# Kernel tuning notes

Measured on AMD Instinct MI355X. Metric: run time of the kernel, lower is better.

## Reference

```python
import jax, jax.numpy as jnp
import numpy as np

N, E, R = 50000, 400000, 500
X_SIZE = 100
G_SIZE = 100
HID = 64
OUT = 64
HEADS = 2
ALPHA = 0.5
NEG_SLOPE = 0.01  # nn.LeakyReLU default and attention slope
EPS = 1e-12       # F.normalize eps


def _l2norm(x, axis):
    return x / jnp.maximum(jnp.linalg.norm(x, axis=axis, keepdims=True), EPS)


def _xavier(key, shape, gain=1.414):
    fan_in, fan_out = shape[-1], int(np.prod(shape[:-1]))
    std = gain * np.sqrt(2.0 / (fan_in + fan_out))
    return jax.random.normal(key, shape, dtype=jnp.float32) * std


def _att_layer(h, g, row, col, etype, W, b, att, out_size):
    # h: [N, D_h], g: [R, D_g], W: [heads*out, 2*D_h+D_g], att: [1, heads, out]
    n = h.shape[0]
    h_ijk = jnp.concatenate([h[row], h[col], g[etype]], axis=1)      # [E, 2D_h+D_g]
    c_ijk = (h_ijk @ W.T + b).reshape(-1, HEADS, out_size)           # [E, H, O]
    a = jnp.sum(att * c_ijk, axis=2, keepdims=True)                  # [E, H, 1]
    e = jnp.exp(jax.nn.leaky_relu(a, NEG_SLOPE))                     # unnormalized (matches torch exp w/o max-sub)
    denom = jax.ops.segment_sum(e, row, num_segments=n)              # [N, H, 1]
    alpha = e / denom[row]
    # self-edge zeros contribute nothing; segment_sum over num_segments=n is equivalent
    return jax.ops.segment_sum(alpha * c_ijk, col, num_segments=n)   # [N, H, O]


def setup_inputs() -> dict:
    key = jax.random.key(0)
    ks = jax.random.split(key, 20)
    x = jax.random.normal(ks[0], (N, X_SIZE), dtype=jnp.float32)
    g = jax.random.normal(ks[1], (R, G_SIZE), dtype=jnp.float32)
    edge_idx = jax.random.randint(ks[2], (2, E), 0, N)
    edge_type = jax.random.randint(ks[3], (E,), 0, R)
    d1 = 2 * X_SIZE + G_SIZE
    d2 = 2 * HID * HEADS + G_SIZE
    inp = {
        "x": x, "g": g, "edge_idx": edge_idx, "edge_type": edge_type,
        "W1i": _xavier(ks[4], (HEADS * HID, d1)), "b1i": jnp.zeros((HEADS * HID,), jnp.float32),
        "a1i": _xavier(ks[5], (1, HEADS, HID)),
        "W1o": _xavier(ks[6], (HEADS * HID, d1)), "b1o": jnp.zeros((HEADS * HID,), jnp.float32),
        "a1o": _xavier(ks[7], (1, HEADS, HID)),
        "W2i": _xavier(ks[8], (HEADS * OUT, d2)), "b2i": jnp.zeros((HEADS * OUT,), jnp.float32),
        "a2i": _xavier(ks[9], (1, HEADS, OUT)),
        "W2o": _xavier(ks[10], (HEADS * OUT, d2)), "b2o": jnp.zeros((HEADS * OUT,), jnp.float32),
        "a2o": _xavier(ks[11], (1, HEADS, OUT)),
        "We": _xavier(ks[12], (HID, X_SIZE)), "be": jnp.zeros((HID,), jnp.float32),
        "Wr": _xavier(ks[13], (HEADS * HID, G_SIZE)), "br": jnp.zeros((HEADS * HID,), jnp.float32),
    }
    return inp


def reference(x, g, edge_idx, edge_type, W1i, b1i, a1i, W1o, b1o, a1o,
              W2i, b2i, a2i, W2o, b2o, a2o, We, be, Wr, br):
    # x = F.normalize(x, dim=1).detach()
    xn = jax.lax.stop_gradient(_l2norm(x, axis=1))
    row, col = edge_idx[0], edge_idx[1]

    h_in = _att_layer(xn, g, row, col, edge_type, W1i, b1i, a1i, HID)
    h_out = _att_layer(xn, g, col, row, edge_type, W1o, b1o, a1o, HID)
    h = jax.nn.leaky_relu(ALPHA * h_in + (1.0 - ALPHA) * h_out, NEG_SLOPE)
    h = _l2norm(h, axis=2)                                # [N, H, HID]
    h = h.transpose(0, 1, 2).reshape(N, HEADS * HID)      # concat heads

    h_in = _att_layer(h, g, row, col, edge_type, W2i, b2i, a2i, OUT)
    h_out = _att_layer(h, g, col, row, edge_type, W2o, b2o, a2o, OUT)
    h = jax.nn.leaky_relu(ALPHA * h_in + (1.0 - ALPHA) * h_out, NEG_SLOPE)
    h = _l2norm(h, axis=2)                                # [N, H, OUT]

    # EntityLayer: Linear(x)[:, None, :] + h  (requires HID == OUT)
    h_prime = (xn @ We.T + be)[:, None, :] + h            # [N, H, OUT]
    h_prime = h_prime.reshape(N, HEADS * OUT)
    h_prime = _l2norm(h_prime, axis=1)                    # (torch dim=2 bug -> last dim)
    # _merge_heads stores mean but returns input unchanged

    g_prime = g @ Wr.T + br                               # [R, HEADS*HID]
    return h_prime, g_prime
```

## Files before the change

kernel.cpp:

```cpp
#include <hip/hip_runtime.h>

typedef unsigned short u16;
typedef unsigned int u32;
typedef short short8v __attribute__((ext_vector_type(8)));
typedef float float4v __attribute__((ext_vector_type(4)));

#define N_NODES 50000
#define E_EDGES 400000
#define R_REL   500
#define NKEYS   100000
#define SCAN_B  98

__device__ __forceinline__ float bl(u32 u){ return __uint_as_float(u << 16); }
__device__ __forceinline__ float bh(u32 u){ return __uint_as_float(u & 0xffff0000u); }
__device__ __forceinline__ u16 f2b(float f){
    u32 u = __float_as_uint(f);
    return (u16)((u + 0x7fffu + ((u >> 16) & 1u)) >> 16);
}
__device__ __forceinline__ u32 pk2(float a, float b){ return (u32)f2b(a) | ((u32)f2b(b) << 16); }
__device__ __forceinline__ float lrelu(float x){ return x > 0.f ? x : 0.01f * x; }

__global__ void k_norm_x(const float* __restrict__ x, u16* __restrict__ xnb){
    int wid = threadIdx.x >> 6, l = threadIdx.x & 63;
    int n = blockIdx.x * 4 + wid;
    if (n >= N_NODES) return;
    float v0 = x[(size_t)n * 100 + l];
    float v1 = (l + 64 < 100) ? x[(size_t)n * 100 + 64 + l] : 0.f;
    float ss = v0 * v0 + v1 * v1;
    #pragma unroll
    for (int m = 32; m; m >>= 1) ss += __shfl_xor(ss, m);
    float s = 1.f / fmaxf(sqrtf(ss), 1e-12f);
    xnb[(size_t)n * 128 + l] = f2b(v0 * s);
    xnb[(size_t)n * 128 + 64 + l] = (l + 64 < 100) ? f2b(v1 * s) : (u16)0;
}

__global__ void k_build_wcat(const float* __restrict__ W1i, const float* __restrict__ W1o,
                             const float* __restrict__ W2i, const float* __restrict__ W2o,
                             const float* __restrict__ We,
                             u16* __restrict__ wc1, u16* __restrict__ wc2){
    int idx = blockIdx.x * blockDim.x + threadIdx.x;
    if (idx < 576 * 128){
        int r = idx >> 7, k = idx & 127;
        float v = 0.f;
        if (r < 512){
            int seg = r >> 7, rr = r & 127;
            const float* W = (seg < 2) ? W1i : W1o;
            int off = (seg & 1) ? 100 : 0;
            if (k < 100) v = W[(size_t)rr * 300 + off + k];
        } else {
            int rr = r - 512;
            if (k < 100) v = We[(size_t)rr * 100 + k];
        }
        wc1[idx] = f2b(v);
    } else if (idx < 576 * 128 + 512 * 128){
        int j = idx - 576 * 128;
        int r = j >> 7, k = j & 127;
        int seg = r >> 7, rr = r & 127;
        const float* W = (seg < 2) ? W2i : W2o;
        int off = (seg & 1) ? 128 : 0;
        wc2[j] = f2b(W[(size_t)rr * 356 + off + k]);
    }
}

__global__ void k_pg(const float* __restrict__ g,
                     const float* __restrict__ W1i, const float* __restrict__ W1o,
                     const float* __restrict__ W2i, const float* __restrict__ W2o,
                     const float* __restrict__ b1i, const float* __restrict__ b1o,
                     const float* __restrict__ b2i, const float* __restrict__ b2o,
                     const float* __restrict__ a1i, const float* __restrict__ a1o,
                     const float* __restrict__ a2i, const float* __restrict__ a2o,
                     float* __restrict__ Pg, float* __restrict__ qg){
    int bid = blockIdx.x;
    int r = bid >> 2, t = bid & 3;
    const float *W, *b, *att; int ld, off;
    if (t == 0){ W = W1i; ld = 300; off = 200; b = b1i; att = a1i; }
    else if (t == 1){ W = W1o; ld = 300; off = 200; b = b1o; att = a1o; }
    else if (t == 2){ W = W2i; ld = 356; off = 256; b = b2i; att = a2i; }
    else { W = W2o; ld = 356; off = 256; b = b2o; att = a2o; }
    __shared__ float gs[100];
    __shared__ float red[128];
    int j = threadIdx.x;
    if (j < 100) gs[j] = g[(size_t)r * 100 + j];
    __syncthreads();
    float acc = b[j];
    #pragma unroll 4
    for (int k = 0; k < 100; ++k) acc += gs[k] * W[(size_t)j * ld + off + k];
    Pg[((size_t)t * R_REL + r) * 128 + j] = acc;
    red[j] = att[j] * acc;
    __syncthreads();
    if (j < 2){
        float s = 0.f;
        for (int k = 0; k < 64; ++k) s += red[j * 64 + k];
        qg[((size_t)t * R_REL + r) * 2 + j] = s;
    }
}

__global__ void k_gprime(const float* __restrict__ g, const float* __restrict__ Wr,
                         const float* __restrict__ br, float* __restrict__ out){
    int r = blockIdx.x, j = threadIdx.x;
    __shared__ float gs[100];
    if (j < 100) gs[j] = g[(size_t)r * 100 + j];
    __syncthreads();
    float acc = br[j];
    #pragma unroll 4
    for (int k = 0; k < 100; ++k) acc += gs[k] * Wr[(size_t)j * 100 + k];
    out[(size_t)N_NODES * 128 + (size_t)r * 128 + j] = acc;
}

__launch_bounds__(256)
__global__ void k_gemm(const u16* __restrict__ A, const u16* __restrict__ W,
                       u16* __restrict__ C, int M, int NN){
    int l = threadIdx.x & 63, w = threadIdx.x >> 6;
    int rb = blockIdx.x * 64 + w * 16;
    int ar = rb + (l & 15); if (ar >= M) ar = M - 1;
    const u16* Ap = A + (size_t)ar * 128 + (l >> 4) * 8;
    short8v a0 = *(const short8v*)(Ap);
    short8v a1 = *(const short8v*)(Ap + 32);
    short8v a2 = *(const short8v*)(Ap + 64);
    short8v a3 = *(const short8v*)(Ap + 96);
    int ntc = NN >> 4;
    for (int nt = 0; nt < ntc; ++nt){
        const u16* Wp = W + (size_t)(nt * 16 + (l & 15)) * 128 + (l >> 4) * 8;
        short8v b0 = *(const short8v*)(Wp);
        short8v b1 = *(const short8v*)(Wp + 32);
        short8v b2 = *(const short8v*)(Wp + 64);
        short8v b3 = *(const short8v*)(Wp + 96);
        float4v acc = {0.f, 0.f, 0.f, 0.f};
        acc = __builtin_amdgcn_mfma_f32_16x16x32_bf16(a0, b0, acc, 0, 0, 0);
        acc = __builtin_amdgcn_mfma_f32_16x16x32_bf16(a1, b1, acc, 0, 0, 0);
        acc = __builtin_amdgcn_mfma_f32_16x16x32_bf16(a2, b2, acc, 0, 0, 0);
        acc = __builtin_amdgcn_mfma_f32_16x16x32_bf16(a3, b3, acc, 0, 0, 0);
        int cc = nt * 16 + (l & 15);
        int rr0 = rb + (l >> 4) * 4;
        #pragma unroll
        for (int r = 0; r < 4; ++r){
            int rr = rr0 + r;
            if (rr < M) C[(size_t)rr * NN + cc] = f2b(acc[r]);
        }
    }
}

__global__ void k_qnode(const u16* __restrict__ NP, int stride,
                        const float* __restrict__ attI, const float* __restrict__ attO,
                        float* __restrict__ q){
    int wid = threadIdx.x >> 6, l = threadIdx.x & 63;
    int n = blockIdx.x * 4 + wid;
    if (n >= N_NODES) return;
    uint4 uv = *(const uint4*)(NP + (size_t)n * stride + (size_t)l * 8);
    int t = l >> 4, h = (l >> 3) & 1;
    const float* att = ((t < 2) ? attI : attO) + h * 64 + (l & 7) * 8;
    float s = bl(uv.x) * att[0] + bh(uv.x) * att[1] + bl(uv.y) * att[2] + bh(uv.y) * att[3]
            + bl(uv.z) * att[4] + bh(uv.z) * att[5] + bl(uv.w) * att[6] + bh(uv.w) * att[7];
    s += __shfl_xor(s, 1); s += __shfl_xor(s, 2); s += __shfl_xor(s, 4);
    if ((l & 7) == 0) q[(size_t)n * 8 + t * 2 + h] = s;
}

__global__ void k_hist(const int* __restrict__ ei, u32* __restrict__ cnt){
    int e = blockIdx.x * blockDim.x + threadIdx.x;
    if (e >= E_EDGES) return;
    atomicAdd(&cnt[ei[E_EDGES + e]], 1u);
    atomicAdd(&cnt[N_NODES + ei[e]], 1u);
}

__launch_bounds__(1024)
__global__ void k_scan1(const u32* __restrict__ cnt, u32* __restrict__ off, u32* __restrict__ bsum){
    __shared__ u32 sh[1024];
    int t = threadIdx.x, b = blockIdx.x, idx = b * 1024 + t;
    u32 v = cnt[idx];
    sh[t] = v; __syncthreads();
    #pragma unroll
    for (int d = 1; d < 1024; d <<= 1){
        u32 add = (t >= d) ? sh[t - d] : 0;
        __syncthreads();
        sh[t] += add;
        __syncthreads();
    }
    off[idx] = sh[t] - v;
    if (t == 1023) bsum[b] = sh[1023];
}

__global__ void k_scan2(u32* __restrict__ bsum){
    if (threadIdx.x == 0){
        u32 run = 0;
        for (int i = 0; i < SCAN_B; ++i){ u32 t = bsum[i]; bsum[i] = run; run += t; }
    }
}

__launch_bounds__(1024)
__global__ void k_scan3(u32* __restrict__ off, const u32* __restrict__ bsum){
    int idx = blockIdx.x * 1024 + threadIdx.x;
    off[idx] += bsum[blockIdx.x];
}

__global__ void k_pos(const int* __restrict__ ei, const int* __restrict__ ety,
                      u32* __restrict__ cur,
                      u32* __restrict__ Pso, u32* __restrict__ Pss){
    int e = blockIdx.x * blockDim.x + threadIdx.x;
    if (e >= E_EDGES) return;
    u32 row = (u32)ei[e], col = (u32)ei[E_EDGES + e];
    u32 etb = (u32)ety[e] << 20;
    u32 pI = atomicAdd(&cur[col], 1u);
    Pso[pI] = row | etb;  Pss[pI] = col;
    u32 pO = atomicAdd(&cur[N_NODES + row], 1u);
    Pso[pO] = col | etb;  Pss[pO] = row;
}

__global__ void k_edgeA(const u32* __restrict__ Pso, const u32* __restrict__ Pss,
                        const float* __restrict__ q,
                        const float* __restrict__ qgI, const float* __restrict__ qgO,
                        float4* __restrict__ ex){
    int p = blockIdx.x * blockDim.x + threadIdx.x;
    if (p >= 2 * E_EDGES) return;
    u32 so = Pso[p], self = Pss[p];
    u32 oth = so & 0xFFFFF, et = so >> 20;
    u32 row, col;
    if (p < E_EDGES){ row = oth; col = self; } else { row = self; col = oth; }
    const float* qr = q + (size_t)row * 8;
    const float* qc = q + (size_t)col * 8;
    float4 r;
    r.x = expf(lrelu(qr[0] + qc[2] + qgI[(size_t)et * 2 + 0]));
    r.y = expf(lrelu(qr[1] + qc[3] + qgI[(size_t)et * 2 + 1]));
    r.z = expf(lrelu(qc[4] + qr[6] + qgO[(size_t)et * 2 + 0]));
    r.w = expf(lrelu(qc[5] + qr[7] + qgO[(size_t)et * 2 + 1]));
    ex[p] = r;
}

__global__ void k_denom(const u32* __restrict__ off, const float4* __restrict__ ex,
                        float* __restrict__ rdI, float* __restrict__ rdO){
    int n = blockIdx.x * blockDim.x + threadIdx.x;
    if (n >= N_NODES) return;
    float s0 = 0.f, s1 = 0.f;
    for (u32 p = off[N_NODES + n]; p < off[N_NODES + n + 1]; ++p){
        float4 v = ex[p]; s0 += v.x; s1 += v.y;
    }
    rdI[(size_t)n * 2 + 0] = (s0 > 0.f) ? 1.f / s0 : 0.f;
    rdI[(size_t)n * 2 + 1] = (s1 > 0.f) ? 1.f / s1 : 0.f;
    float t0 = 0.f, t1 = 0.f;
    for (u32 p = off[n]; p < off[n + 1]; ++p){
        float4 v = ex[p]; t0 += v.z; t1 += v.w;
    }
    rdO[(size_t)n * 2 + 0] = (t0 > 0.f) ? 1.f / t0 : 0.f;
    rdO[(size_t)n * 2 + 1] = (t1 > 0.f) ? 1.f / t1 : 0.f;
}

__launch_bounds__(256)
__global__ void k_agg(const u32* __restrict__ off,
                      const u32* __restrict__ Pso, const float4* __restrict__ ex,
                      const u16* __restrict__ NP, int stride,
                      const float* __restrict__ PgI, const float* __restrict__ PgO,
                      const float* __restrict__ rdI, const float* __restrict__ rdO,
                      int final_stage,
                      const u16* __restrict__ NP1, const float* __restrict__ be,
                      u16* __restrict__ h1b, float* __restrict__ out){
    int wid = threadIdx.x >> 6, l = threadIdx.x & 63;
    int n = blockIdx.x * 4 + wid;
    if (n >= N_NODES) return;
    int h = l >> 5, d0 = l * 2;
    const u16* selfP = NP + (size_t)n * stride;
    u32 pbi = *(const u32*)(selfP + 128 + d0);
    u32 pbo = *(const u32*)(selfP + 384 + d0);

    float a0 = 0.f, a1 = 0.f, sai = 0.f;
    {
        u32 s0 = off[n], deg = off[n + 1] - s0;
        for (u32 base = 0; base < deg; base += 64){
            u32 k = base + (u32)l;
            u32 so = 0u; float ex0 = 0.f, ex1 = 0.f;
            if (k < deg){
                so = Pso[s0 + k];
                float2 e2 = *(const float2*)((const char*)ex + (size_t)(s0 + k) * 16);
                ex0 = e2.x; ex1 = e2.y;
            }
            int cnt = (int)((deg - base < 64u) ? (deg - base) : 64u);
            for (int c = 0; c < cnt; c += 8){
                float wj[8]; u32 pa[8]; float2 gv[8];
                #pragma unroll
                for (int j = 0; j < 8; ++j){
                    u32 s = __shfl(so, c + j);
                    float e0 = __shfl(ex0, c + j);
                    float e1 = __shfl(ex1, c + j);
                    float e = h ? e1 : e0;
                    u32 oth = s & 0xFFFFFu, et = s >> 20;
                    pa[j] = *(const u32*)(NP + (size_t)oth * stride + d0);
                    gv[j] = *(const float2*)(PgI + (size_t)et * 128 + d0);
                    wj[j] = e * rdI[(size_t)oth * 2 + h];
                }
                #pragma unroll
                for (int j = 0; j < 8; ++j){
                    a0 += wj[j] * (bl(pa[j]) + gv[j].x);
                    a1 += wj[j] * (bh(pa[j]) + gv[j].y);
                    sai += wj[j];
                }
            }
        }
    }
    a0 += sai * bl(pbi);
    a1 += sai * bh(pbi);

    float b0 = 0.f, b1 = 0.f, sao = 0.f;
    {
        u32 s0 = off[N_NODES + n], deg = off[N_NODES + n + 1] - s0;
        for (u32 base = 0; base < deg; base += 64){
            u32 k = base + (u32)l;
            u32 so = 0u; float ex0 = 0.f, ex1 = 0.f;
            if (k < deg){
                so = Pso[s0 + k];
                float2 e2 = *(const float2*)((const char*)ex + (size_t)(s0 + k) * 16 + 8);
                ex0 = e2.x; ex1 = e2.y;
            }
            int cnt = (int)((deg - base < 64u) ? (deg - base) : 64u);
            for (int c = 0; c < cnt; c += 8){
                float wj[8]; u32 pa[8]; float2 gv[8];
                #pragma unroll
                for (int j = 0; j < 8; ++j){
                    u32 s = __shfl(so, c + j);
                    float e0 = __shfl(ex0, c + j);
                    float e1 = __shfl(ex1, c + j);
                    float e = h ? e1 : e0;
                    u32 oth = s & 0xFFFFFu, et = s >> 20;
                    pa[j] = *(const u32*)(NP + (size_t)oth * stride + 256 + d0);
                    gv[j] = *(const float2*)(PgO + (size_t)et * 128 + d0);
                    wj[j] = e * rdO[(size_t)oth * 2 + h];
                }
                #pragma unroll
                for (int j = 0; j < 8; ++j){
                    b0 += wj[j] * (bl(pa[j]) + gv[j].x);
                    b1 += wj[j] * (bh(pa[j]) + gv[j].y);
                    sao += wj[j];
                }
            }
        }
    }
    b0 += sao * bl(pbo);
    b1 += sao * bh(pbo);

    float vx = lrelu(0.5f * (a0 + b0));
    float vy = lrelu(0.5f * (a1 + b1));
    float ss = vx * vx + vy * vy;
    #pragma unroll
    for (int m = 16; m; m >>= 1) ss += __shfl_xor(ss, m);
    float s2 = 1.f / fmaxf(sqrtf(ss), 1e-12f);
    if (!final_stage){
        *(u32*)(h1b + (size_t)n * 128 + d0) = pk2(vx * s2, vy * s2);
    } else {
        float h20 = vx * s2, h21 = vy * s2;
        int o0 = d0 & 63;
        u32 ue = *(const u32*)(NP1 + (size_t)n * 576 + 512 + o0);
        float hp0 = bl(ue) + be[o0] + h20;
        float hp1 = bh(ue) + be[o0 + 1] + h21;
        float st = hp0 * hp0 + hp1 * hp1;
        #pragma unroll
        for (int m = 32; m; m >>= 1) st += __shfl_xor(st, m);
        float s = 1.f / fmaxf(sqrtf(st), 1e-12f);
        float2 o; o.x = hp0 * s; o.y = hp1 * s;
        *(float2*)(out + (size_t)n * 128 + d0) = o;
    }
}

extern "C" void kernel_launch(void* const* d_in, const int* in_sizes, int n_in,
                              void* d_out, int out_size, void* d_ws, size_t ws_size,
                              hipStream_t stream){
    const float* x   = (const float*)d_in[0];
    const float* g   = (const float*)d_in[1];
    const int*   ei  = (const int*)d_in[2];
    const int*   ety = (const int*)d_in[3];
    const float* W1i = (const float*)d_in[4];
    const float* b1i = (const float*)d_in[5];
    const float* a1i = (const float*)d_in[6];
    const float* W1o = (const float*)d_in[7];
    const float* b1o = (const float*)d_in[8];
    const float* a1o = (const float*)d_in[9];
    const float* W2i = (const float*)d_in[10];
    const float* b2i = (const float*)d_in[11];
    const float* a2i = (const float*)d_in[12];
    const float* W2o = (const float*)d_in[13];
    const float* b2o = (const float*)d_in[14];
    const float* a2o = (const float*)d_in[15];
    const float* We  = (const float*)d_in[16];
    const float* be  = (const float*)d_in[17];
    const float* Wr  = (const float*)d_in[18];
    const float* br  = (const float*)d_in[19];
    float* out = (float*)d_out;

    char* ws = (char*)d_ws;
    size_t off_b = 0;
    auto carve = [&](size_t bytes) -> char* {
        char* p = ws + off_b;
        off_b += (bytes + 255) & ~(size_t)255;
        return p;
    };
    u16*    xnb  = (u16*)carve((size_t)N_NODES * 128 * 2);
    u16*    wc1  = (u16*)carve((size_t)576 * 128 * 2);
    u16*    wc2  = (u16*)carve((size_t)512 * 128 * 2);
    u16*    NP1  = (u16*)carve((size_t)N_NODES * 576 * 2);
    u16*    NP2  = (u16*)carve((size_t)N_NODES * 512 * 2);
    u16*    h1b  = (u16*)carve((size_t)N_NODES * 128 * 2);
    float*  q    = (float*)carve((size_t)N_NODES * 8 * 4);
    float*  Pg   = (float*)carve((size_t)4 * R_REL * 128 * 4);
    float*  qg   = (float*)carve((size_t)4 * R_REL * 2 * 4);
    u32*    cnt  = (u32*)carve((size_t)SCAN_B * 1024 * 4);
    u32*    offA = (u32*)carve((size_t)SCAN_B * 1024 * 4);
    u32*    cur  = (u32*)carve((size_t)NKEYS * 4);
    u32*    bsum = (u32*)carve((size_t)SCAN_B * 4);
    u32*    Pso  = (u32*)carve((size_t)2 * E_EDGES * 4);
    u32*    Pss  = (u32*)carve((size_t)2 * E_EDGES * 4);
    float4* ex   = (float4*)carve((size_t)2 * E_EDGES * 16);
    float*  rdI  = (float*)carve((size_t)N_NODES * 2 * 4);
    float*  rdO  = (float*)carve((size_t)N_NODES * 2 * 4);

    hipMemsetAsync(cnt, 0, (size_t)SCAN_B * 1024 * 4, stream);
    k_hist<<<1563, 256, 0, stream>>>(ei, cnt);
    k_scan1<<<SCAN_B, 1024, 0, stream>>>(cnt, offA, bsum);
    k_scan2<<<1, 64, 0, stream>>>(bsum);
    k_scan3<<<SCAN_B, 1024, 0, stream>>>(offA, bsum);
    hipMemcpyAsync(cur, offA, (size_t)NKEYS * 4, hipMemcpyDeviceToDevice, stream);
    k_pos<<<1563, 256, 0, stream>>>(ei, ety, cur, Pso, Pss);

    k_norm_x<<<12500, 256, 0, stream>>>(x, xnb);
    k_build_wcat<<<544, 256, 0, stream>>>(W1i, W1o, W2i, W2o, We, wc1, wc2);
    k_pg<<<2000, 128, 0, stream>>>(g, W1i, W1o, W2i, W2o, b1i, b1o, b2i, b2o,
                                   a1i, a1o, a2i, a2o, Pg, qg);
    k_gprime<<<500, 128, 0, stream>>>(g, Wr, br, out);

    k_gemm<<<782, 256, 0, stream>>>(xnb, wc1, NP1, N_NODES, 576);
    k_qnode<<<12500, 256, 0, stream>>>(NP1, 576, a1i, a1o, q);
    k_edgeA<<<3125, 256, 0, stream>>>(Pso, Pss, q, qg, qg + R_REL * 2, ex);
    k_denom<<<196, 256, 0, stream>>>(offA, ex, rdI, rdO);
    k_agg<<<12500, 256, 0, stream>>>(offA, Pso, ex, NP1, 576, Pg, Pg + R_REL * 128,
                                     rdI, rdO, 0, NP1, be, h1b, out);

    k_gemm<<<782, 256, 0, stream>>>(h1b, wc2, NP2, N_NODES, 512);
    k_qnode<<<12500, 256, 0, stream>>>(NP2, 512, a2i, a2o, q);
    k_edgeA<<<3125, 256, 0, stream>>>(Pso, Pss, q, qg + 2 * R_REL * 2, qg + 3 * R_REL * 2, ex);
    k_denom<<<196, 256, 0, stream>>>(offA, ex, rdI, rdO);
    k_agg<<<12500, 256, 0, stream>>>(offA, Pso, ex, NP2, 512, Pg + 2 * R_REL * 128,
                                     Pg + 3 * R_REL * 128, rdI, rdO, 1, NP1, be, h1b, out);
}
```

Before: 461.0 us.

## Split node projections into per-segment planes and interleave in/out aggregation loops

New measurement: 470.5 us. 1.02x slower.

```diff
diff --git a/kernel.cpp b/kernel.cpp
--- a/kernel.cpp
+++ b/kernel.cpp
@@ -10,6 +10,7 @@
 #define R_REL   500
 #define NKEYS   100000
 #define SCAN_B  98
+#define SEG     ((size_t)N_NODES * 128)
 
 __device__ __forceinline__ float bl(u32 u){ return __uint_as_float(u << 16); }
 __device__ __forceinline__ float bh(u32 u){ return __uint_as_float(u & 0xffff0000u); }
@@ -109,7 +110,7 @@
 
 __launch_bounds__(256)
 __global__ void k_gemm(const u16* __restrict__ A, const u16* __restrict__ W,
-                       u16* __restrict__ C, int M, int NN){
+                       u16* __restrict__ NPt, int M, int NN){
     int l = threadIdx.x & 63, w = threadIdx.x >> 6;
     int rb = blockIdx.x * 64 + w * 16;
     int ar = rb + (l & 15); if (ar >= M) ar = M - 1;
@@ -131,23 +132,27 @@
         acc = __builtin_amdgcn_mfma_f32_16x16x32_bf16(a2, b2, acc, 0, 0, 0);
         acc = __builtin_amdgcn_mfma_f32_16x16x32_bf16(a3, b3, acc, 0, 0, 0);
         int cc = nt * 16 + (l & 15);
+        int seg = cc >> 7;
         int rr0 = rb + (l >> 4) * 4;
         #pragma unroll
         for (int r = 0; r < 4; ++r){
             int rr = rr0 + r;
-            if (rr < M) C[(size_t)rr * NN + cc] = f2b(acc[r]);
+            if (rr < M){
+                if (seg < 4) NPt[(size_t)seg * SEG + (size_t)rr * 128 + (cc & 127)] = f2b(acc[r]);
+                else         NPt[4 * SEG + (size_t)rr * 64 + (cc & 63)] = f2b(acc[r]);
+            }
         }
     }
 }
 
-__global__ void k_qnode(const u16* __restrict__ NP, int stride,
+__global__ void k_qnode(const u16* __restrict__ NPt,
                         const float* __restrict__ attI, const float* __restrict__ attO,
                         float* __restrict__ q){
     int wid = threadIdx.x >> 6, l = threadIdx.x & 63;
     int n = blockIdx.x * 4 + wid;
     if (n >= N_NODES) return;
-    uint4 uv = *(const uint4*)(NP + (size_t)n * stride + (size_t)l * 8);
     int t = l >> 4, h = (l >> 3) & 1;
+    uint4 uv = *(const uint4*)(NPt + (size_t)t * SEG + (size_t)n * 128 + (l & 15) * 8);
     const float* att = ((t < 2) ? attI : attO) + h * 64 + (l & 7) * 8;
     float s = bl(uv.x) * att[0] + bh(uv.x) * att[1] + bl(uv.y) * att[2] + bh(uv.y) * att[3]
             + bl(uv.z) * att[4] + bh(uv.z) * att[5] + bl(uv.w) * att[6] + bh(uv.w) * att[7];
@@ -246,91 +251,96 @@
 __launch_bounds__(256)
 __global__ void k_agg(const u32* __restrict__ off,
                       const u32* __restrict__ Pso, const float4* __restrict__ ex,
-                      const u16* __restrict__ NP, int stride,
+                      const u16* __restrict__ NPt,
                       const float* __restrict__ PgI, const float* __restrict__ PgO,
                       const float* __restrict__ rdI, const float* __restrict__ rdO,
                       int final_stage,
-                      const u16* __restrict__ NP1, const float* __restrict__ be,
+                      const u16* __restrict__ NPt1, const float* __restrict__ be,
                       u16* __restrict__ h1b, float* __restrict__ out){
     int wid = threadIdx.x >> 6, l = threadIdx.x & 63;
     int n = blockIdx.x * 4 + wid;
     if (n >= N_NODES) return;
     int h = l >> 5, d0 = l * 2;
-    const u16* selfP = NP + (size_t)n * stride;
-    u32 pbi = *(const u32*)(selfP + 128 + d0);
-    u32 pbo = *(const u32*)(selfP + 384 + d0);
+    const u16* PaI = NPt;
+    const u16* PbI = NPt + SEG;
+    const u16* PaO = NPt + 2 * SEG;
+    const u16* PbO = NPt + 3 * SEG;
+    u32 pbi = *(const u32*)(PbI + (size_t)n * 128 + d0);
+    u32 pbo = *(const u32*)(PbO + (size_t)n * 128 + d0);
+
+    u32 sI = off[n],           degI = off[n + 1] - sI;
+    u32 sO = off[N_NODES + n], degO = off[N_NODES + n + 1] - sO;
+    u32 degM = degI > degO ? degI : degO;
 
     float a0 = 0.f, a1 = 0.f, sai = 0.f;
-    {
-        u32 s0 = off[n], deg = off[n + 1] - s0;
-        for (u32 base = 0; base < deg; base += 64){
-            u32 k = base + (u32)l;
-            u32 so = 0u; float ex0 = 0.f, ex1 = 0.f;
-            if (k < deg){
-                so = Pso[s0 + k];
-                float2 e2 = *(const float2*)((const char*)ex + (size_t)(s0 + k) * 16);
-                ex0 = e2.x; ex1 = e2.y;
-            }
-            int cnt = (int)((deg - base < 64u) ? (deg - base) : 64u);
-            for (int c = 0; c < cnt; c += 8){
-                float wj[8]; u32 pa[8]; float2 gv[8];
+    float b0 = 0.f, b1 = 0.f, sao = 0.f;
+
+    for (u32 base = 0; base < degM; base += 64){
+        u32 soI = 0u; float eI0 = 0.f, eI1 = 0.f;
+        if (base + (u32)l < degI){
+            u32 idx = sI + base + (u32)l;
+            soI = Pso[idx];
+            float2 e2 = *(const float2*)((const char*)ex + (size_t)idx * 16);
+            eI0 = e2.x; eI1 = e2.y;
+        }
+        u32 soO = 0u; float eO0 = 0.f, eO1 = 0.f;
+        if (base + (u32)l < degO){
+            u32 idx = sO + base + (u32)l;
+            soO = Pso[idx];
+            float2 e2 = *(const float2*)((const char*)ex + (size_t)idx * 16 + 8);
+            eO0 = e2.x; eO1 = e2.y;
+        }
+        int cntI = (int)((degI > base) ? ((degI - base < 64u) ? degI - base : 64u) : 0u);
+        int cntO = (int)((degO > base) ? ((degO - base < 64u) ? degO - base : 64u) : 0u);
+        int cmax = cntI > cntO ? cntI : cntO;
+        for (int c = 0; c < cmax; c += 8){
+            float wI[8]; u32 paI[8]; float2 gvI[8];
+            float wO[8]; u32 paO[8]; float2 gvO[8];
+            bool doI = c < cntI, doO = c < cntO;
+            if (doI){
                 #pragma unroll
                 for (int j = 0; j < 8; ++j){
-                    u32 s = __shfl(so, c + j);
-                    float e0 = __shfl(ex0, c + j);
-                    float e1 = __shfl(ex1, c + j);
-                    float e = h ? e1 : e0;
+                    u32 s = __shfl(soI, c + j);
+                    float e0 = __shfl(eI0, c + j);
+                    float e1 = __shfl(eI1, c + j);
                     u32 oth = s & 0xFFFFFu, et = s >> 20;
-                    pa[j] = *(const u32*)(NP + (size_t)oth * stride + d0);
-                    gv[j] = *(const float2*)(PgI + (size_t)et * 128 + d0);
-                    wj[j] = e * rdI[(size_t)oth * 2 + h];
+                    paI[j] = *(const u32*)(PaI + (size_t)oth * 128 + d0);
+                    gvI[j] = *(const float2*)(PgI + (size_t)et * 128 + d0);
+                    wI[j] = (h ? e1 : e0) * rdI[(size_t)oth * 2 + h];
                 }
+            }
+            if (doO){
                 #pragma unroll
                 for (int j = 0; j < 8; ++j){
-                    a0 += wj[j] * (bl(pa[j]) + gv[j].x);
-                    a1 += wj[j] * (bh(pa[j]) + gv[j].y);
-                    sai += wj[j];
+                    u32 s = __shfl(soO, c + j);
+                    float e0 = __shfl(eO0, c + j);
+                    float e1 = __shfl(eO1, c + j);
+                    u32 oth = s & 0xFFFFFu, et = s >> 20;
+                    paO[j] = *(const u32*)(PaO + (size_t)oth * 128 + d0);
+                    gvO[j] = *(const float2*)(PgO + (size_t)et * 128 + d0);
+                    wO[j] = (h ? e1 : e0) * rdO[(size_t)oth * 2 + h];
+                }
+            }
+            if (doI){
+                #pragma unroll
+                for (int j = 0; j < 8; ++j){
+                    a0 += wI[j] * (bl(paI[j]) + gvI[j].x);
+                    a1 += wI[j] * (bh(paI[j]) + gvI[j].y);
+                    sai += wI[j];
+                }
+            }
+            if (doO){
+                #pragma unroll
+                for (int j = 0; j < 8; ++j){
+                    b0 += wO[j] * (bl(paO[j]) + gvO[j].x);
+                    b1 += wO[j] * (bh(paO[j]) + gvO[j].y);
+                    sao += wO[j];
                 }
             }
         }
     }
     a0 += sai * bl(pbi);
     a1 += sai * bh(pbi);
-
-    float b0 = 0.f, b1 = 0.f, sao = 0.f;
-    {
-        u32 s0 = off[N_NODES + n], deg = off[N_NODES + n + 1] - s0;
-        for (u32 base = 0; base < deg; base += 64){
-            u32 k = base + (u32)l;
-            u32 so = 0u; float ex0 = 0.f, ex1 = 0.f;
-            if (k < deg){
-                so = Pso[s0 + k];
-                float2 e2 = *(const float2*)((const char*)ex + (size_t)(s0 + k) * 16 + 8);
-                ex0 = e2.x; ex1 = e2.y;
-            }
-            int cnt = (int)((deg - base < 64u) ? (deg - base) : 64u);
-            for (int c = 0; c < cnt; c += 8){
-                float wj[8]; u32 pa[8]; float2 gv[8];
-                #pragma unroll
-                for (int j = 0; j < 8; ++j){
-                    u32 s = __shfl(so, c + j);
-                    float e0 = __shfl(ex0, c + j);
-                    float e1 = __shfl(ex1, c + j);
-                    float e = h ? e1 : e0;
-                    u32 oth = s & 0xFFFFFu, et = s >> 20;
-                    pa[j] = *(const u32*)(NP + (size_t)oth * stride + 256 + d0);
-                    gv[j] = *(const float2*)(PgO + (size_t)et * 128 + d0);
-                    wj[j] = e * rdO[(size_t)oth * 2 + h];
-                }
-                #pragma unroll
-                for (int j = 0; j < 8; ++j){
-                    b0 += wj[j] * (bl(pa[j]) + gv[j].x);
-                    b1 += wj[j] * (bh(pa[j]) + gv[j].y);
-                    sao += wj[j];
-                }
-            }
-        }
-    }
     b0 += sao * bl(pbo);
     b1 += sao * bh(pbo);
 
@@ -345,7 +355,7 @@
     } else {
         float h20 = vx * s2, h21 = vy * s2;
         int o0 = d0 & 63;
-        u32 ue = *(const u32*)(NP1 + (size_t)n * 576 + 512 + o0);
+        u32 ue = *(const u32*)(NPt1 + 4 * SEG + (size_t)n * 64 + o0);
         float hp0 = bl(ue) + be[o0] + h20;
         float hp1 = bh(ue) + be[o0 + 1] + h21;
         float st = hp0 * hp0 + hp1 * hp1;
@@ -392,8 +402,8 @@
     u16*    xnb  = (u16*)carve((size_t)N_NODES * 128 * 2);
     u16*    wc1  = (u16*)carve((size_t)576 * 128 * 2);
     u16*    wc2  = (u16*)carve((size_t)512 * 128 * 2);
-    u16*    NP1  = (u16*)carve((size_t)N_NODES * 576 * 2);
-    u16*    NP2  = (u16*)carve((size_t)N_NODES * 512 * 2);
+    u16*    NPt1 = (u16*)carve((SEG * 4 + (size_t)N_NODES * 64) * 2);
+    u16*    NPt2 = (u16*)carve(SEG * 4 * 2);
     u16*    h1b  = (u16*)carve((size_t)N_NODES * 128 * 2);
     float*  q    = (float*)carve((size_t)N_NODES * 8 * 4);
     float*  Pg   = (float*)carve((size_t)4 * R_REL * 128 * 4);
@@ -422,17 +432,17 @@
                                    a1i, a1o, a2i, a2o, Pg, qg);
     k_gprime<<<500, 128, 0, stream>>>(g, Wr, br, out);
 
-    k_gemm<<<782, 256, 0, stream>>>(xnb, wc1, NP1, N_NODES, 576);
-    k_qnode<<<12500, 256, 0, stream>>>(NP1, 576, a1i, a1o, q);
+    k_gemm<<<782, 256, 0, stream>>>(xnb, wc1, NPt1, N_NODES, 576);
+    k_qnode<<<12500, 256, 0, stream>>>(NPt1, a1i, a1o, q);
     k_edgeA<<<3125, 256, 0, stream>>>(Pso, Pss, q, qg, qg + R_REL * 2, ex);
     k_denom<<<196, 256, 0, stream>>>(offA, ex, rdI, rdO);
-    k_agg<<<12500, 256, 0, stream>>>(offA, Pso, ex, NP1, 576, Pg, Pg + R_REL * 128,
-                                     rdI, rdO, 0, NP1, be, h1b, out);
-
-    k_gemm<<<782, 256, 0, stream>>>(h1b, wc2, NP2, N_NODES, 512);
-    k_qnode<<<12500, 256, 0, stream>>>(NP2, 512, a2i, a2o, q);
+    k_agg<<<12500, 256, 0, stream>>>(offA, Pso, ex, NPt1, Pg, Pg + R_REL * 128,
+                                     rdI, rdO, 0, NPt1, be, h1b, out);
+
+    k_gemm<<<782, 256, 0, stream>>>(h1b, wc2, NPt2, N_NODES, 512);
+    k_qnode<<<12500, 256, 0, stream>>>(NPt2, a2i, a2o, q);
     k_edgeA<<<3125, 256, 0, stream>>>(Pso, Pss, q, qg + 2 * R_REL * 2, qg + 3 * R_REL * 2, ex);
     k_denom<<<196, 256, 0, stream>>>(offA, ex, rdI, rdO);
-    k_agg<<<12500, 256, 0, stream>>>(offA, Pso, ex, NP2, 512, Pg + 2 * R_REL * 128,
-                                     Pg + 3 * R_REL * 128, rdI, rdO, 1, NP1, be, h1b, out);
-}
+    k_agg<<<12500, 256, 0, stream>>>(offA, Pso, ex, NPt2, Pg + 2 * R_REL * 128,
+                                     Pg + 3 * R_REL * 128, rdI, rdO, 1, NPt1, be, h1b, out);
+}
```

## Split node projections into per-segment planes and separate edge exp arrays

Applied to the files above, without the earlier changes.

New measurement: 451.3 us. 2.1% less time.

```diff
diff --git a/kernel.cpp b/kernel.cpp
--- a/kernel.cpp
+++ b/kernel.cpp
@@ -10,6 +10,7 @@
 #define R_REL   500
 #define NKEYS   100000
 #define SCAN_B  98
+#define SEG     ((size_t)N_NODES * 128)
 
 __device__ __forceinline__ float bl(u32 u){ return __uint_as_float(u << 16); }
 __device__ __forceinline__ float bh(u32 u){ return __uint_as_float(u & 0xffff0000u); }
@@ -109,7 +110,7 @@
 
 __launch_bounds__(256)
 __global__ void k_gemm(const u16* __restrict__ A, const u16* __restrict__ W,
-                       u16* __restrict__ C, int M, int NN){
+                       u16* __restrict__ NPt, int M, int NN){
     int l = threadIdx.x & 63, w = threadIdx.x >> 6;
     int rb = blockIdx.x * 64 + w * 16;
     int ar = rb + (l & 15); if (ar >= M) ar = M - 1;
@@ -131,23 +132,27 @@
         acc = __builtin_amdgcn_mfma_f32_16x16x32_bf16(a2, b2, acc, 0, 0, 0);
         acc = __builtin_amdgcn_mfma_f32_16x16x32_bf16(a3, b3, acc, 0, 0, 0);
         int cc = nt * 16 + (l & 15);
+        int seg = cc >> 7;
         int rr0 = rb + (l >> 4) * 4;
         #pragma unroll
         for (int r = 0; r < 4; ++r){
             int rr = rr0 + r;
-            if (rr < M) C[(size_t)rr * NN + cc] = f2b(acc[r]);
+            if (rr < M){
+                if (seg < 4) NPt[(size_t)seg * SEG + (size_t)rr * 128 + (cc & 127)] = f2b(acc[r]);
+                else         NPt[4 * SEG + (size_t)rr * 64 + (cc & 63)] = f2b(acc[r]);
+            }
         }
     }
 }
 
-__global__ void k_qnode(const u16* __restrict__ NP, int stride,
+__global__ void k_qnode(const u16* __restrict__ NPt,
                         const float* __restrict__ attI, const float* __restrict__ attO,
                         float* __restrict__ q){
     int wid = threadIdx.x >> 6, l = threadIdx.x & 63;
     int n = blockIdx.x * 4 + wid;
     if (n >= N_NODES) return;
-    uint4 uv = *(const uint4*)(NP + (size_t)n * stride + (size_t)l * 8);
     int t = l >> 4, h = (l >> 3) & 1;
+    uint4 uv = *(const uint4*)(NPt + (size_t)t * SEG + (size_t)n * 128 + (l & 15) * 8);
     const float* att = ((t < 2) ? attI : attO) + h * 64 + (l & 7) * 8;
     float s = bl(uv.x) * att[0] + bh(uv.x) * att[1] + bl(uv.y) * att[2] + bh(uv.y) * att[3]
             + bl(uv.z) * att[4] + bh(uv.z) * att[5] + bl(uv.w) * att[6] + bh(uv.w) * att[7];
@@ -208,7 +213,7 @@
 __global__ void k_edgeA(const u32* __restrict__ Pso, const u32* __restrict__ Pss,
                         const float* __restrict__ q,
                         const float* __restrict__ qgI, const float* __restrict__ qgO,
-                        float4* __restrict__ ex){
+                        float2* __restrict__ exI, float2* __restrict__ exO){
     int p = blockIdx.x * blockDim.x + threadIdx.x;
     if (p >= 2 * E_EDGES) return;
     u32 so = Pso[p], self = Pss[p];
@@ -217,27 +222,29 @@
     if (p < E_EDGES){ row = oth; col = self; } else { row = self; col = oth; }
     const float* qr = q + (size_t)row * 8;
     const float* qc = q + (size_t)col * 8;
-    float4 r;
-    r.x = expf(lrelu(qr[0] + qc[2] + qgI[(size_t)et * 2 + 0]));
-    r.y = expf(lrelu(qr[1] + qc[3] + qgI[(size_t)et * 2 + 1]));
-    r.z = expf(lrelu(qc[4] + qr[6] + qgO[(size_t)et * 2 + 0]));
-    r.w = expf(lrelu(qc[5] + qr[7] + qgO[(size_t)et * 2 + 1]));
-    ex[p] = r;
-}
-
-__global__ void k_denom(const u32* __restrict__ off, const float4* __restrict__ ex,
+    float2 ri, ro;
+    ri.x = expf(lrelu(qr[0] + qc[2] + qgI[(size_t)et * 2 + 0]));
+    ri.y = expf(lrelu(qr[1] + qc[3] + qgI[(size_t)et * 2 + 1]));
+    ro.x = expf(lrelu(qc[4] + qr[6] + qgO[(size_t)et * 2 + 0]));
+    ro.y = expf(lrelu(qc[5] + qr[7] + qgO[(size_t)et * 2 + 1]));
+    exI[p] = ri;
+    exO[p] = ro;
+}
+
+__global__ void k_denom(const u32* __restrict__ off,
+                        const float2* __restrict__ exI, const float2* __restrict__ exO,
                         float* __restrict__ rdI, float* __restrict__ rdO){
     int n = blockIdx.x * blockDim.x + threadIdx.x;
     if (n >= N_NODES) return;
     float s0 = 0.f, s1 = 0.f;
     for (u32 p = off[N_NODES + n]; p < off[N_NODES + n + 1]; ++p){
-        float4 v = ex[p]; s0 += v.x; s1 += v.y;
+        float2 v = exI[p]; s0 += v.x; s1 += v.y;
     }
     rdI[(size_t)n * 2 + 0] = (s0 > 0.f) ? 1.f / s0 : 0.f;
     rdI[(size_t)n * 2 + 1] = (s1 > 0.f) ? 1.f / s1 : 0.f;
     float t0 = 0.f, t1 = 0.f;
     for (u32 p = off[n]; p < off[n + 1]; ++p){
-        float4 v = ex[p]; t0 += v.z; t1 += v.w;
+        float2 v = exO[p]; t0 += v.x; t1 += v.y;
     }
     rdO[(size_t)n * 2 + 0] = (t0 > 0.f) ? 1.f / t0 : 0.f;
     rdO[(size_t)n * 2 + 1] = (t1 > 0.f) ? 1.f / t1 : 0.f;
@@ -245,31 +252,40 @@
 
 __launch_bounds__(256)
 __global__ void k_agg(const u32* __restrict__ off,
-                      const u32* __restrict__ Pso, const float4* __restrict__ ex,
-                      const u16* __restrict__ NP, int stride,
+                      const u32* __restrict__ Pso,
+                      const float2* __restrict__ exI, const float2* __restrict__ exO,
+                      const u16* __restrict__ NPt,
                       const float* __restrict__ PgI, const float* __restrict__ PgO,
                       const float* __restrict__ rdI, const float* __restrict__ rdO,
                       int final_stage,
-                      const u16* __restrict__ NP1, const float* __restrict__ be,
+                      const u16* __restrict__ NPt1, const float* __restrict__ be,
                       u16* __restrict__ h1b, float* __restrict__ out){
     int wid = threadIdx.x >> 6, l = threadIdx.x & 63;
     int n = blockIdx.x * 4 + wid;
     if (n >= N_NODES) return;
     int h = l >> 5, d0 = l * 2;
-    const u16* selfP = NP + (size_t)n * stride;
-    u32 pbi = *(const u32*)(selfP + 128 + d0);
-    u32 pbo = *(const u32*)(selfP + 384 + d0);
+    const u16* PaI = NPt;
+    const u16* PbI = NPt + SEG;
+    const u16* PaO = NPt + 2 * SEG;
+    const u16* PbO = NPt + 3 * SEG;
+    u32 pbi = *(const u32*)(PbI + (size_t)n * 128 + d0);
+    u32 pbo = *(const u32*)(PbO + (size_t)n * 128 + d0);
 
     float a0 = 0.f, a1 = 0.f, sai = 0.f;
     {
         u32 s0 = off[n], deg = off[n + 1] - s0;
         for (u32 base = 0; base < deg; base += 64){
             u32 k = base + (u32)l;
-            u32 so = 0u; float ex0 = 0.f, ex1 = 0.f;
+            u32 so = 0u; float w0 = 0.f, w1 = 0.f;
             if (k < deg){
-                so = Pso[s0 + k];
-                float2 e2 = *(const float2*)((const char*)ex + (size_t)(s0 + k) * 16);
-                ex0 = e2.x; ex1 = e2.y;
+                u32 idx = s0 + k;
+                so = __builtin_nontemporal_load(Pso + idx);
+                const float* ep = (const float*)exI + (size_t)idx * 2;
+                float e0 = __builtin_nontemporal_load(ep);
+                float e1 = __builtin_nontemporal_load(ep + 1);
+                u32 oth = so & 0xFFFFFu;
+                float2 rd2 = *(const float2*)(rdI + (size_t)oth * 2);
+                w0 = e0 * rd2.x; w1 = e1 * rd2.y;
             }
             int cnt = (int)((deg - base < 64u) ? (deg - base) : 64u);
             for (int c = 0; c < cnt; c += 8){
@@ -277,13 +293,12 @@
                 #pragma unroll
                 for (int j = 0; j < 8; ++j){
                     u32 s = __shfl(so, c + j);
-                    float e0 = __shfl(ex0, c + j);
-                    float e1 = __shfl(ex1, c + j);
-                    float e = h ? e1 : e0;
+                    float v0 = __shfl(w0, c + j);
+                    float v1 = __shfl(w1, c + j);
                     u32 oth = s & 0xFFFFFu, et = s >> 20;
-                    pa[j] = *(const u32*)(NP + (size_t)oth * stride + d0);
+                    pa[j] = *(const u32*)(PaI + (size_t)oth * 128 + d0);
                     gv[j] = *(const float2*)(PgI + (size_t)et * 128 + d0);
-                    wj[j] = e * rdI[(size_t)oth * 2 + h];
+                    wj[j] = h ? v1 : v0;
                 }
                 #pragma unroll
                 for (int j = 0; j < 8; ++j){
@@ -302,11 +317,16 @@
         u32 s0 = off[N_NODES + n], deg = off[N_NODES + n + 1] - s0;
         for (u32 base = 0; base < deg; base += 64){
             u32 k = base + (u32)l;
-            u32 so = 0u; float ex0 = 0.f, ex1 = 0.f;
+            u32 so = 0u; float w0 = 0.f, w1 = 0.f;
             if (k < deg){
-                so = Pso[s0 + k];
-                float2 e2 = *(const float2*)((const char*)ex + (size_t)(s0 + k) * 16 + 8);
-                ex0 = e2.x; ex1 = e2.y;
+                u32 idx = s0 + k;
+                so = __builtin_nontemporal_load(Pso + idx);
+                const float* ep = (const float*)exO + (size_t)idx * 2;
+                float e0 = __builtin_nontemporal_load(ep);
+                float e1 = __builtin_nontemporal_load(ep + 1);
+                u32 oth = so & 0xFFFFFu;
+                float2 rd2 = *(const float2*)(rdO + (size_t)oth * 2);
+                w0 = e0 * rd2.x; w1 = e1 * rd2.y;
             }
             int cnt = (int)((deg - base < 64u) ? (deg - base) : 64u);
             for (int c = 0; c < cnt; c += 8){
@@ -314,13 +334,12 @@
                 #pragma unroll
                 for (int j = 0; j < 8; ++j){
                     u32 s = __shfl(so, c + j);
-                    float e0 = __shfl(ex0, c + j);
-                    float e1 = __shfl(ex1, c + j);
-                    float e = h ? e1 : e0;
+                    float v0 = __shfl(w0, c + j);
+                    float v1 = __shfl(w1, c + j);
                     u32 oth = s & 0xFFFFFu, et = s >> 20;
-                    pa[j] = *(const u32*)(NP + (size_t)oth * stride + 256 + d0);
+                    pa[j] = *(const u32*)(PaO + (size_t)oth * 128 + d0);
                     gv[j] = *(const float2*)(PgO + (size_t)et * 128 + d0);
-                    wj[j] = e * rdO[(size_t)oth * 2 + h];
+                    wj[j] = h ? v1 : v0;
                 }
                 #pragma unroll
                 for (int j = 0; j < 8; ++j){
@@ -345,7 +364,7 @@
     } else {
         float h20 = vx * s2, h21 = vy * s2;
         int o0 = d0 & 63;
-        u32 ue = *(const u32*)(NP1 + (size_t)n * 576 + 512 + o0);
+        u32 ue = *(const u32*)(NPt1 + 4 * SEG + (size_t)n * 64 + o0);
         float hp0 = bl(ue) + be[o0] + h20;
         float hp1 = bh(ue) + be[o0 + 1] + h21;
         float st = hp0 * hp0 + hp1 * hp1;
@@ -392,8 +411,8 @@
     u16*    xnb  = (u16*)carve((size_t)N_NODES * 128 * 2);
     u16*    wc1  = (u16*)carve((size_t)576 * 128 * 2);
     u16*    wc2  = (u16*)carve((size_t)512 * 128 * 2);
-    u16*    NP1  = (u16*)carve((size_t)N_NODES * 576 * 2);
-    u16*    NP2  = (u16*)carve((size_t)N_NODES * 512 * 2);
+    u16*    NPt1 = (u16*)carve((SEG * 4 + (size_t)N_NODES * 64) * 2);
+    u16*    NPt2 = (u16*)carve(SEG * 4 * 2);
     u16*    h1b  = (u16*)carve((size_t)N_NODES * 128 * 2);
     float*  q    = (float*)carve((size_t)N_NODES * 8 * 4);
     float*  Pg   = (float*)carve((size_t)4 * R_REL * 128 * 4);
@@ -404,7 +423,8 @@
     u32*    bsum = (u32*)carve((size_t)SCAN_B * 4);
     u32*    Pso  = (u32*)carve((size_t)2 * E_EDGES * 4);
     u32*    Pss  = (u32*)carve((size_t)2 * E_EDGES * 4);
-    float4* ex   = (float4*)carve((size_t)2 * E_EDGES * 16);
+    float2* exI  = (float2*)carve((size_t)2 * E_EDGES * 8);
+    float2* exO  = (float2*)carve((size_t)2 * E_EDGES * 8);
     float*  rdI  = (float*)carve((size_t)N_NODES * 2 * 4);
     float*  rdO  = (float*)carve((size_t)N_NODES * 2 * 4);
 
@@ -422,17 +442,18 @@
                                    a1i, a1o, a2i, a2o, Pg, qg);
     k_gprime<<<500, 128, 0, stream>>>(g, Wr, br, out);
 
-    k_gemm<<<782, 256, 0, stream>>>(xnb, wc1, NP1, N_NODES, 576);
-    k_qnode<<<12500, 256, 0, stream>>>(NP1, 576, a1i, a1o, q);
-    k_edgeA<<<3125, 256, 0, stream>>>(Pso, Pss, q, qg, qg + R_REL * 2, ex);
-    k_denom<<<196, 256, 0, stream>>>(offA, ex, rdI, rdO);
-    k_agg<<<12500, 256, 0, stream>>>(offA, Pso, ex, NP1, 576, Pg, Pg + R_REL * 128,
-                                     rdI, rdO, 0, NP1, be, h1b, out);
-
-    k_gemm<<<782, 256, 0, stream>>>(h1b, wc2, NP2, N_NODES, 512);
-    k_qnode<<<12500, 256, 0, stream>>>(NP2, 512, a2i, a2o, q);
-    k_edgeA<<<3125, 256, 0, stream>>>(Pso, Pss, q, qg + 2 * R_REL * 2, qg + 3 * R_REL * 2, ex);
-    k_denom<<<196, 256, 0, stream>>>(offA, ex, rdI, rdO);
-    k_agg<<<12500, 256, 0, stream>>>(offA, Pso, ex, NP2, 512, Pg + 2 * R_REL * 128,
-                                     Pg + 3 * R_REL * 128, rdI, rdO, 1, NP1, be, h1b, out);
-}
+    k_gemm<<<782, 256, 0, stream>>>(xnb, wc1, NPt1, N_NODES, 576);
+    k_qnode<<<12500, 256, 0, stream>>>(NPt1, a1i, a1o, q);
+    k_edgeA<<<3125, 256, 0, stream>>>(Pso, Pss, q, qg, qg + R_REL * 2, exI, exO);
+    k_denom<<<196, 256, 0, stream>>>(offA, exI, exO, rdI, rdO);
+    k_agg<<<12500, 256, 0, stream>>>(offA, Pso, exI, exO, NPt1, Pg, Pg + R_REL * 128,
+                                     rdI, rdO, 0, NPt1, be, h1b, out);
+
+    k_gemm<<<782, 256, 0, stream>>>(h1b, wc2, NPt2, N_NODES, 512);
+    k_qnode<<<12500, 256, 0, stream>>>(NPt2, a2i, a2o, q);
+    k_edgeA<<<3125, 256, 0, stream>>>(Pso, Pss, q, qg + 2 * R_REL * 2, qg + 3 * R_REL * 2,
+                                      exI, exO);
+    k_denom<<<196, 256, 0, stream>>>(offA, exI, exO, rdI, rdO);
+    k_agg<<<12500, 256, 0, stream>>>(offA, Pso, exI, exO, NPt2, Pg + 2 * R_REL * 128,
+                                     Pg + 3 * R_REL * 128, rdI, rdO, 1, NPt1, be, h1b, out);
+}
```
